# Kernel optimization log

Measured on AMD Instinct MI355X. Metric: run time of the kernel, lower is better.

## Reference

```python
import jax, jax.numpy as jnp
import numpy as np
from jax import lax

C, NORI, NROT, K, PAD = 256, 8, 2, 3, 1
B, H, W = 16, 64, 64
EPS = 1e-5


def setup_inputs() -> dict:
    key = jax.random.key(0)
    k1, k2, k3 = jax.random.split(key, 3)
    x = jax.random.normal(k1, (B, C, H, W), dtype=jnp.float32)
    # rotate_arf() output: [nRot*C, nOri*C, K, K]
    weight_all = jax.random.normal(k2, (NROT * C, NORI * C, K, K), dtype=jnp.float32) * 0.02
    bias_all = jax.random.normal(k3, (NROT * C,), dtype=jnp.float32) * 0.02
    alpha = jnp.float32(1.0)
    gamma = jnp.ones((C,), dtype=jnp.float32)
    beta = jnp.zeros((C,), dtype=jnp.float32)
    return {"x": x, "weight_all": weight_all, "bias_all": bias_all,
            "alpha": alpha, "gamma": gamma, "beta": beta}


def _forward(x, weight_all, bias_all, alpha, gamma, beta):
    # Loop of nOri*nRot convs over the same x with different weight blocks,
    # all accumulated into one [B,C,H,W] tensor == single conv with summed blocks
    # (conv is linear in the weights): fused form of the original loop.
    W_eff = weight_all.reshape(NROT, C, NORI, C, K, K).sum(axis=(0, 2))  # [C, C, K, K]
    b_eff = bias_all.reshape(NROT, C).sum(axis=0) * NORI                 # [C]
    d_sum = lax.conv_general_dilated(
        x, W_eff, window_strides=(1, 1), padding=[(PAD, PAD), (PAD, PAD)],
        dimension_numbers=("NCHW", "OIHW", "NCHW"))
    d_sum = d_sum + b_eff[None, :, None, None]
    d_mean = d_sum / float(NORI * NROT)
    out = x + alpha * d_mean
    # BatchNorm2d, training mode: biased batch stats over (B, H, W)
    mean = out.mean(axis=(0, 2, 3))
    var = ((out - mean[None, :, None, None]) ** 2).mean(axis=(0, 2, 3))
    inv = lax.rsqrt(var + EPS)
    y = (out - mean[None, :, None, None]) * (gamma * inv)[None, :, None, None] \
        + beta[None, :, None, None]
    return y


def reference(x, weight_all, bias_all, alpha, gamma, beta):
    return _forward(x, weight_all, bias_all, alpha, gamma, beta)
```

## Files before the change

kernel.cpp:

```cpp
#include <hip/hip_runtime.h>
#include <stdint.h>

typedef __attribute__((__ext_vector_type__(8))) __bf16 bf16x8;
typedef __attribute__((__ext_vector_type__(4))) float  f32x4;

#define XT_OFF    0ul
#define WT_OFF    33554432ul
#define BEFF_OFF  34734080ul
#define ZERO_OFF  34737152ul
#define STATS_OFF 34737408ul
#define V_OFF     35651584ul
#define WS_NEED   (V_OFF + 33554432ul)

__device__ inline void gload_lds16(const void* g, void* l) {
  __builtin_amdgcn_global_load_lds((const __attribute__((address_space(1))) void*)g,
                                   (__attribute__((address_space(3))) void*)l,
                                   16, 0, 0);
}

__global__ void k_prep(const float* __restrict__ w, const float* __restrict__ bias,
                       const float* __restrict__ alpha_p, __bf16* __restrict__ Wt,
                       float* __restrict__ beff, float* __restrict__ zerob,
                       float* __restrict__ statsG,
                       const float* __restrict__ x, __bf16* __restrict__ xT) {
  __shared__ __bf16 lds[64 * 258];
  if (blockIdx.x < 256) {
    const int co = blockIdx.x;
    const int ci = threadIdx.x;
    float a[9];
#pragma unroll
    for (int t = 0; t < 9; ++t) a[t] = 0.f;
#pragma unroll
    for (int r = 0; r < 2; ++r)
#pragma unroll
      for (int o = 0; o < 8; ++o) {
        const float* p = w + ((size_t)(r * 256 + co) * 2048 + (size_t)(o * 256 + ci)) * 9;
#pragma unroll
        for (int t = 0; t < 9; ++t) a[t] += p[t];
      }
    const float sc = alpha_p[0] * 0.0625f;
    const int s = ci >> 6, cis = ci & 63;
#pragma unroll
    for (int t = 0; t < 9; ++t)
      Wt[(size_t)(t * 4 + s) * 16384 + co * 64 + cis] = (__bf16)(a[t] * sc);
    if (ci == 0) beff[co] = (bias[co] + bias[256 + co]) * 8.0f * sc;
    if (blockIdx.x == 0) {
      statsG[ci] = 0.f; statsG[256 + ci] = 0.f;
      if (ci < 64) zerob[ci] = 0.f;
    }
  } else {
    int bh = blockIdx.x - 256;
    int b = bh >> 6, h = bh & 63;
    int t = threadIdx.x;
    int w2 = t & 63, cg = t >> 6;
    const float* xb = x + ((size_t)b * 16384 + h) * 64;
#pragma unroll 4
    for (int cb = 0; cb < 256; cb += 4) {
      int ci = cb + cg;
      lds[w2 * 258 + ci] = (__bf16)xb[(size_t)ci * 4096 + w2];
    }
    __syncthreads();
    const uint32_t* l32 = (const uint32_t*)lds;
    uint32_t* o32 = (uint32_t*)(xT + ((size_t)b * 64 + h) * 64 * 256);
    int c2 = t & 127, wg = t >> 7;
    for (int w0 = 0; w0 < 64; w0 += 2) {
      int ww = w0 + wg;
      o32[ww * 128 + c2] = l32[ww * 129 + c2];
    }
  }
}

#define A_BYTES 51200
#define B_BYTES 32768

__global__ __launch_bounds__(1024) void k_conv(
    const float* __restrict__ x, const __bf16* __restrict__ xT,
    const __bf16* __restrict__ Wt, const float* __restrict__ beff,
    const __bf16* __restrict__ zerob, float* __restrict__ out,
    float* __restrict__ statsG, __bf16* __restrict__ vout, int use_v16)
{
  __shared__ __align__(16) char lds[A_BYTES + 3 * B_BYTES + 2048];
  const int bb   = blockIdx.x >> 4;
  const int ho0  = (blockIdx.x & 15) << 2;
  const int tid  = threadIdx.x;
  const int lane = tid & 63;
  const int wid  = tid >> 6;
  const int wr   = wid >> 2;
  const int wc   = wid & 3;
  const int l15  = lane & 15;

  f32x4 acc[4][4];
#pragma unroll
  for (int i = 0; i < 4; ++i)
#pragma unroll
    for (int j = 0; j < 4; ++j)
#pragma unroll
      for (int r = 0; r < 4; ++r) acc[i][j][r] = 0.f;

  const char* zb = (const char*)zerob;

  int boff[4][2];
#pragma unroll
  for (int j = 0; j < 4; ++j)
#pragma unroll
    for (int kk = 0; kk < 2; ++kk) {
      const int co     = (wc << 6) + (j << 4) + l15;
      const int ci_off = (kk << 5) + ((lane >> 4) << 3);
      boff[j][kk] = ((co << 7) + (ci_off << 1)) ^ ((co & 7) << 4);
    }
  const int bl = lane >> 3;
  const int bsrcLane = (bl << 7) + (((lane & 7) ^ (bl & 7)) << 4);

  auto stageA = [&](int s) {
    const int ci0 = s << 6;
    for (int t = wid; t < 50; t += 16) {
      const int ch = (t << 3) + (lane >> 3);
      const int r  = ch / 66;
      const int c  = ch - r * 66;
      const int ir = ho0 - 1 + r;
      const int ic = c - 1;
      const int k  = (lane & 7) ^ (ch & 7);
      const char* src;
      if (ch < 396 && ir >= 0 && ir < 64 && ic >= 0 && ic < 64)
        src = (const char*)(xT + ((((size_t)bb << 6) + ir) * 64 + ic) * 256 + ci0 + (k << 3));
      else
        src = zb + (k << 4);
      gload_lds16(src, lds + (t << 10));
    }
  };

  auto stageB = [&](int ph, int bi) {
    char* buf = lds + A_BYTES + bi * B_BYTES;
    const int s2 = ph / 9, tp = ph - s2 * 9;
    const char* wsrc = (const char*)Wt + ((size_t)(tp * 4 + s2) << 15) + bsrcLane;
    gload_lds16(wsrc + (wid << 10), buf + (wid << 10));
    gload_lds16(wsrc + ((wid + 16) << 10), buf + ((wid + 16) << 10));
  };

  stageA(0);
  stageB(0, 0);
  stageB(1, 1);
  asm volatile("s_waitcnt vmcnt(0)" ::: "memory");
  __builtin_amdgcn_s_barrier();
  asm volatile("" ::: "memory");

  int s = 0, tap = 0, bcur = 0;
  for (int p = 0; p < 36; ++p) {
    if (p + 2 < 36) {
      int bnx = bcur + 2; if (bnx >= 3) bnx -= 3;
      stageB(p + 2, bnx);
    }
    const int dh = (tap >= 6) ? 2 : (tap >= 3 ? 1 : 0);
    const int dw = tap - dh * 3;
    const char* Bb = lds + A_BYTES + bcur * B_BYTES;
    __builtin_amdgcn_s_setprio(1);
#pragma unroll
    for (int kk = 0; kk < 2; ++kk) {
      const int ci_off = (kk << 5) + ((lane >> 4) << 3);
      bf16x8 av[4];
#pragma unroll
      for (int i = 0; i < 4; ++i) {
        const int pos = (wr + dh) * 66 + (i << 4) + l15 + dw;
        const int off = ((pos << 7) + (ci_off << 1)) ^ ((pos & 7) << 4);
        av[i] = *(const bf16x8*)(lds + off);
      }
#pragma unroll
      for (int j = 0; j < 4; ++j) {
        const bf16x8 bv = *(const bf16x8*)(Bb + boff[j][kk]);
#pragma unroll
        for (int i = 0; i < 4; ++i)
          acc[i][j] = __builtin_amdgcn_mfma_f32_16x16x32_bf16(av[i], bv, acc[i][j], 0, 0, 0);
      }
    }
    __builtin_amdgcn_s_setprio(0);

    if (tap == 8 && s < 3) {
      asm volatile("s_waitcnt vmcnt(0)" ::: "memory");
      __builtin_amdgcn_s_barrier();
      asm volatile("" ::: "memory");
      stageA(s + 1);
      asm volatile("s_waitcnt vmcnt(0)" ::: "memory");
      __builtin_amdgcn_s_barrier();
      asm volatile("" ::: "memory");
    } else if (p + 2 < 36) {
      asm volatile("s_waitcnt vmcnt(2)" ::: "memory");
      __builtin_amdgcn_s_barrier();
      asm volatile("" ::: "memory");
    } else if (p < 35) {
      asm volatile("s_waitcnt vmcnt(0)" ::: "memory");
      __builtin_amdgcn_s_barrier();
      asm volatile("" ::: "memory");
    }
    if (++tap == 9) { tap = 0; ++s; }
    if (++bcur == 3) bcur = 0;
  }

  __syncthreads();
  float* lstat = (float*)(lds + 32768);
  if (tid < 512) lstat[tid] = 0.f;
  __syncthreads();

  char* wreg = lds + wid * 2048;
  const int wq = lane >> 4;
  const int ho = ho0 + wr;
  const int xorco = (l15 & 7) << 4;
#pragma unroll
  for (int j = 0; j < 4; ++j) {
    const int co = (wc << 6) + (j << 4) + l15;
    const float be = beff[co];
    const size_t base = ((((size_t)bb << 8) + (size_t)co) << 12) + (ho << 6);
    float r1 = 0.f, r2 = 0.f;
#pragma unroll
    for (int i = 0; i < 4; ++i) {
      const int w0 = (i << 4) + (wq << 2);
      const float4 xv = *(const float4*)(x + base + w0);
      float4 v;
      v.x = acc[i][j][0] + xv.x + be;
      v.y = acc[i][j][1] + xv.y + be;
      v.z = acc[i][j][2] + xv.z + be;
      v.w = acc[i][j][3] + xv.w + be;
      r1 += v.x + v.y + v.z + v.w;
      r2 += v.x * v.x + v.y * v.y + v.z * v.z + v.w * v.w;
      if (use_v16) {
        union { __bf16 h[4]; uint64_t u; } pk;
        pk.h[0] = (__bf16)v.x; pk.h[1] = (__bf16)v.y;
        pk.h[2] = (__bf16)v.z; pk.h[3] = (__bf16)v.w;
        const int wa = (l15 << 7) + (i << 5) + (wq << 3);
        *(uint64_t*)(wreg + (wa ^ xorco)) = pk.u;
      } else {
        *(float4*)(out + base + w0) = v;
      }
    }
    r1 += __shfl_xor(r1, 16); r2 += __shfl_xor(r2, 16);
    r1 += __shfl_xor(r1, 32); r2 += __shfl_xor(r2, 32);
    if (lane < 16) {
      atomicAdd(&lstat[co], r1);
      atomicAdd(&lstat[256 + co], r2);
    }
    if (use_v16) {
      asm volatile("s_waitcnt lgkmcnt(0)" ::: "memory");
#pragma unroll
      for (int t2 = 0; t2 < 2; ++t2) {
        const int co_r = lane >> 2;
        const int ch   = (lane & 3) + (t2 << 2);
        const int ra   = (co_r << 7) + (ch << 4);
        const uint4 pv = *(const uint4*)(wreg + (ra ^ ((co_r & 7) << 4)));
        const int co_g = (wc << 6) + (j << 4) + co_r;
        const size_t oi = ((((size_t)bb << 8) + (size_t)co_g) << 12) + (ho << 6) + (ch << 3);
        *(uint4*)(vout + oi) = pv;
      }
      asm volatile("s_waitcnt lgkmcnt(0)" ::: "memory");
    }
  }
  __syncthreads();
  if (tid < 512) atomicAdd(&statsG[tid], lstat[tid]);
}

__global__ void k_apply_v16(const __bf16* __restrict__ v, float* __restrict__ out,
                            const float* __restrict__ statsG,
                            const float* __restrict__ gamma,
                            const float* __restrict__ beta) {
  __shared__ float ssc[256], ssh[256];
  const int t = threadIdx.x;
  {
    const float mean = statsG[t] * (1.f / 65536.f);
    const float var  = statsG[256 + t] * (1.f / 65536.f) - mean * mean;
    const float inv  = rsqrtf(var + 1e-5f);
    const float sc   = gamma[t] * inv;
    ssc[t] = sc;
    ssh[t] = beta[t] - mean * sc;
  }
  __syncthreads();
  const uint4* vp = (const uint4*)v;
  for (size_t g = (size_t)blockIdx.x * 256 + t; g < 2097152ul; g += (size_t)gridDim.x * 256) {
    const int co = (int)((g >> 9) & 255);
    const uint4 pv = vp[g];
    const float sc = ssc[co], sh = ssh[co];
    float4 y0, y1;
    y0.x = __uint_as_float((pv.x & 0xffffu) << 16) * sc + sh;
    y0.y = __uint_as_float(pv.x & 0xffff0000u) * sc + sh;
    y0.z = __uint_as_float((pv.y & 0xffffu) << 16) * sc + sh;
    y0.w = __uint_as_float(pv.y & 0xffff0000u) * sc + sh;
    y1.x = __uint_as_float((pv.z & 0xffffu) << 16) * sc + sh;
    y1.y = __uint_as_float(pv.z & 0xffff0000u) * sc + sh;
    y1.z = __uint_as_float((pv.w & 0xffffu) << 16) * sc + sh;
    y1.w = __uint_as_float(pv.w & 0xffff0000u) * sc + sh;
    float4* op = (float4*)(out + g * 8);
    op[0] = y0;
    op[1] = y1;
  }
}

__global__ void k_apply_f32(float* __restrict__ out, const float* __restrict__ statsG,
                            const float* __restrict__ gamma,
                            const float* __restrict__ beta) {
  __shared__ float ssc[256], ssh[256];
  const int t = threadIdx.x;
  {
    const float mean = statsG[t] * (1.f / 65536.f);
    const float var  = statsG[256 + t] * (1.f / 65536.f) - mean * mean;
    const float inv  = rsqrtf(var + 1e-5f);
    const float sc   = gamma[t] * inv;
    ssc[t] = sc;
    ssh[t] = beta[t] - mean * sc;
  }
  __syncthreads();
  float4* op = (float4*)out;
  for (size_t g = (size_t)blockIdx.x * 256 + t; g < 4194304ul; g += (size_t)gridDim.x * 256) {
    const int co = (int)((g >> 10) & 255);
    float4 y = op[g];
    const float sc = ssc[co], sh = ssh[co];
    y.x = y.x * sc + sh; y.y = y.y * sc + sh;
    y.z = y.z * sc + sh; y.w = y.w * sc + sh;
    op[g] = y;
  }
}

extern "C" void kernel_launch(void* const* d_in, const int* in_sizes, int n_in,
                              void* d_out, int out_size, void* d_ws, size_t ws_size,
                              hipStream_t stream) {
  const float* x     = (const float*)d_in[0];
  const float* wall  = (const float*)d_in[1];
  const float* bias  = (const float*)d_in[2];
  const float* alpha = (const float*)d_in[3];
  const float* gamma = (const float*)d_in[4];
  const float* beta  = (const float*)d_in[5];
  float* out = (float*)d_out;

  char* ws = (char*)d_ws;
  __bf16* xT     = (__bf16*)(ws + XT_OFF);
  __bf16* Wt     = (__bf16*)(ws + WT_OFF);
  float*  beff   = (float*)(ws + BEFF_OFF);
  float*  zerob  = (float*)(ws + ZERO_OFF);
  float*  statsG = (float*)(ws + STATS_OFF);
  __bf16* vbuf   = (__bf16*)(ws + V_OFF);
  const int use_v16 = (ws_size >= WS_NEED) ? 1 : 0;

  k_prep<<<1280, 256, 0, stream>>>(wall, bias, alpha, Wt, beff, zerob, statsG, x, xT);
  k_conv<<<256, 1024, 0, stream>>>(x, xT, Wt, beff, (const __bf16*)zerob, out,
                                   statsG, vbuf, use_v16);
  if (use_v16)
    k_apply_v16<<<2048, 256, 0, stream>>>(vbuf, out, statsG, gamma, beta);
  else
    k_apply_f32<<<2048, 256, 0, stream>>>(out, statsG, gamma, beta);
}
```

Measured before the change: 122.7 us.

## Split conv output channels across two 512-thread blocks, drop weight multi-buffering

The conv kernel now runs 512 blocks of 512 threads, each handling half of the 256 output channels for a 4-row tile. Adjacent block IDs are paired so both halves share the same input tile in cache. The triple-buffered weight prefetch is replaced by a single weight buffer that is loaded synchronously each tap. This shrinks LDS per block so more blocks can be resident and more of the GPU is used. The cost is that the input tile is loaded twice and global-load latency is no longer hidden behind the MFMA work.

```diff
diff --git a/kernel.cpp b/kernel.cpp
--- a/kernel.cpp
+++ b/kernel.cpp
@@ -71,22 +71,25 @@
 }
 
 #define A_BYTES 51200
-#define B_BYTES 32768
-
-__global__ __launch_bounds__(1024) void k_conv(
+#define B_BYTES 16384
+
+__global__ __launch_bounds__(512, 4) void k_conv(
     const float* __restrict__ x, const __bf16* __restrict__ xT,
     const __bf16* __restrict__ Wt, const float* __restrict__ beff,
     const __bf16* __restrict__ zerob, float* __restrict__ out,
     float* __restrict__ statsG, __bf16* __restrict__ vout, int use_v16)
 {
-  __shared__ __align__(16) char lds[A_BYTES + 3 * B_BYTES + 2048];
-  const int bb   = blockIdx.x >> 4;
-  const int ho0  = (blockIdx.x & 15) << 2;
+  __shared__ __align__(16) char lds[A_BYTES + B_BYTES + 1024];
+  const int u    = blockIdx.x;
+  const int ch   = (u >> 3) & 1;
+  const int pairid = (u & 7) | ((u >> 4) << 3);
+  const int bb   = pairid >> 4;
+  const int ho0  = (pairid & 15) << 2;
   const int tid  = threadIdx.x;
   const int lane = tid & 63;
   const int wid  = tid >> 6;
-  const int wr   = wid >> 2;
-  const int wc   = wid & 3;
+  const int wr   = wid >> 1;
+  const int wc   = wid & 1;
   const int l15  = lane & 15;
 
   f32x4 acc[4][4];
@@ -104,24 +107,24 @@
   for (int j = 0; j < 4; ++j)
 #pragma unroll
     for (int kk = 0; kk < 2; ++kk) {
-      const int co     = (wc << 6) + (j << 4) + l15;
+      const int col    = (wc << 6) + (j << 4) + l15;
       const int ci_off = (kk << 5) + ((lane >> 4) << 3);
-      boff[j][kk] = ((co << 7) + (ci_off << 1)) ^ ((co & 7) << 4);
+      boff[j][kk] = ((col << 7) + (ci_off << 1)) ^ ((col & 7) << 4);
     }
   const int bl = lane >> 3;
   const int bsrcLane = (bl << 7) + (((lane & 7) ^ (bl & 7)) << 4);
 
   auto stageA = [&](int s) {
     const int ci0 = s << 6;
-    for (int t = wid; t < 50; t += 16) {
-      const int ch = (t << 3) + (lane >> 3);
-      const int r  = ch / 66;
-      const int c  = ch - r * 66;
+    for (int t = wid; t < 50; t += 8) {
+      const int chk = (t << 3) + (lane >> 3);
+      const int r  = chk / 66;
+      const int c  = chk - r * 66;
       const int ir = ho0 - 1 + r;
       const int ic = c - 1;
-      const int k  = (lane & 7) ^ (ch & 7);
+      const int k  = (lane & 7) ^ (chk & 7);
       const char* src;
-      if (ch < 396 && ir >= 0 && ir < 64 && ic >= 0 && ic < 64)
+      if (chk < 396 && ir >= 0 && ir < 64 && ic >= 0 && ic < 64)
         src = (const char*)(xT + ((((size_t)bb << 6) + ir) * 64 + ic) * 256 + ci0 + (k << 3));
       else
         src = zb + (k << 4);
@@ -129,30 +132,25 @@
     }
   };
 
-  auto stageB = [&](int ph, int bi) {
-    char* buf = lds + A_BYTES + bi * B_BYTES;
+  auto stageB = [&](int ph) {
+    char* buf = lds + A_BYTES;
     const int s2 = ph / 9, tp = ph - s2 * 9;
-    const char* wsrc = (const char*)Wt + ((size_t)(tp * 4 + s2) << 15) + bsrcLane;
+    const char* wsrc = (const char*)Wt + ((size_t)(tp * 4 + s2) << 15) + (ch << 14) + bsrcLane;
     gload_lds16(wsrc + (wid << 10), buf + (wid << 10));
-    gload_lds16(wsrc + ((wid + 16) << 10), buf + ((wid + 16) << 10));
+    gload_lds16(wsrc + ((wid + 8) << 10), buf + ((wid + 8) << 10));
   };
 
-  stageA(0);
-  stageB(0, 0);
-  stageB(1, 1);
-  asm volatile("s_waitcnt vmcnt(0)" ::: "memory");
-  __builtin_amdgcn_s_barrier();
-  asm volatile("" ::: "memory");
-
-  int s = 0, tap = 0, bcur = 0;
+  int s = 0, tap = 0;
   for (int p = 0; p < 36; ++p) {
-    if (p + 2 < 36) {
-      int bnx = bcur + 2; if (bnx >= 3) bnx -= 3;
-      stageB(p + 2, bnx);
-    }
+    if (tap == 0) stageA(s);
+    stageB(p);
+    asm volatile("s_waitcnt vmcnt(0)" ::: "memory");
+    __builtin_amdgcn_s_barrier();
+    asm volatile("" ::: "memory");
+
     const int dh = (tap >= 6) ? 2 : (tap >= 3 ? 1 : 0);
     const int dw = tap - dh * 3;
-    const char* Bb = lds + A_BYTES + bcur * B_BYTES;
+    const char* Bb = lds + A_BYTES;
     __builtin_amdgcn_s_setprio(1);
 #pragma unroll
     for (int kk = 0; kk < 2; ++kk) {
@@ -173,31 +171,16 @@
       }
     }
     __builtin_amdgcn_s_setprio(0);
-
-    if (tap == 8 && s < 3) {
-      asm volatile("s_waitcnt vmcnt(0)" ::: "memory");
-      __builtin_amdgcn_s_barrier();
-      asm volatile("" ::: "memory");
-      stageA(s + 1);
-      asm volatile("s_waitcnt vmcnt(0)" ::: "memory");
-      __builtin_amdgcn_s_barrier();
-      asm volatile("" ::: "memory");
-    } else if (p + 2 < 36) {
-      asm volatile("s_waitcnt vmcnt(2)" ::: "memory");
-      __builtin_amdgcn_s_barrier();
-      asm volatile("" ::: "memory");
-    } else if (p < 35) {
-      asm volatile("s_waitcnt vmcnt(0)" ::: "memory");
-      __builtin_amdgcn_s_barrier();
-      asm volatile("" ::: "memory");
-    }
+    asm volatile("" ::: "memory");
+    __builtin_amdgcn_s_barrier();
+    asm volatile("" ::: "memory");
+
     if (++tap == 9) { tap = 0; ++s; }
-    if (++bcur == 3) bcur = 0;
-  }
-
-  __syncthreads();
-  float* lstat = (float*)(lds + 32768);
-  if (tid < 512) lstat[tid] = 0.f;
+  }
+
+  __syncthreads();
+  float* lstat = (float*)(lds + A_BYTES + B_BYTES);
+  if (tid < 256) lstat[tid] = 0.f;
   __syncthreads();
 
   char* wreg = lds + wid * 2048;
@@ -206,9 +189,10 @@
   const int xorco = (l15 & 7) << 4;
 #pragma unroll
   for (int j = 0; j < 4; ++j) {
-    const int co = (wc << 6) + (j << 4) + l15;
-    const float be = beff[co];
-    const size_t base = ((((size_t)bb << 8) + (size_t)co) << 12) + (ho << 6);
+    const int col = (wc << 6) + (j << 4) + l15;
+    const int cog = (ch << 7) + col;
+    const float be = beff[cog];
+    const size_t base = ((((size_t)bb << 8) + (size_t)cog) << 12) + (ho << 6);
     float r1 = 0.f, r2 = 0.f;
 #pragma unroll
     for (int i = 0; i < 4; ++i) {
@@ -222,11 +206,11 @@
       r1 += v.x + v.y + v.z + v.w;
       r2 += v.x * v.x + v.y * v.y + v.z * v.z + v.w * v.w;
       if (use_v16) {
-        union { __bf16 h[4]; uint64_t u; } pk;
+        union { __bf16 h[4]; uint64_t u64; } pk;
         pk.h[0] = (__bf16)v.x; pk.h[1] = (__bf16)v.y;
         pk.h[2] = (__bf16)v.z; pk.h[3] = (__bf16)v.w;
         const int wa = (l15 << 7) + (i << 5) + (wq << 3);
-        *(uint64_t*)(wreg + (wa ^ xorco)) = pk.u;
+        *(uint64_t*)(wreg + (wa ^ xorco)) = pk.u64;
       } else {
         *(float4*)(out + base + w0) = v;
       }
@@ -234,26 +218,29 @@
     r1 += __shfl_xor(r1, 16); r2 += __shfl_xor(r2, 16);
     r1 += __shfl_xor(r1, 32); r2 += __shfl_xor(r2, 32);
     if (lane < 16) {
-      atomicAdd(&lstat[co], r1);
-      atomicAdd(&lstat[256 + co], r2);
+      atomicAdd(&lstat[col], r1);
+      atomicAdd(&lstat[128 + col], r2);
     }
     if (use_v16) {
       asm volatile("s_waitcnt lgkmcnt(0)" ::: "memory");
 #pragma unroll
       for (int t2 = 0; t2 < 2; ++t2) {
         const int co_r = lane >> 2;
-        const int ch   = (lane & 3) + (t2 << 2);
-        const int ra   = (co_r << 7) + (ch << 4);
+        const int chk  = (lane & 3) + (t2 << 2);
+        const int ra   = (co_r << 7) + (chk << 4);
         const uint4 pv = *(const uint4*)(wreg + (ra ^ ((co_r & 7) << 4)));
-        const int co_g = (wc << 6) + (j << 4) + co_r;
-        const size_t oi = ((((size_t)bb << 8) + (size_t)co_g) << 12) + (ho << 6) + (ch << 3);
+        const int co_g = (ch << 7) + (wc << 6) + (j << 4) + co_r;
+        const size_t oi = ((((size_t)bb << 8) + (size_t)co_g) << 12) + (ho << 6) + (chk << 3);
         *(uint4*)(vout + oi) = pv;
       }
       asm volatile("s_waitcnt lgkmcnt(0)" ::: "memory");
     }
   }
   __syncthreads();
-  if (tid < 512) atomicAdd(&statsG[tid], lstat[tid]);
+  if (tid < 256) {
+    const int c = tid & 127, part = tid >> 7;
+    atomicAdd(&statsG[part * 256 + (ch << 7) + c], lstat[part * 128 + c]);
+  }
 }
 
 __global__ void k_apply_v16(const __bf16* __restrict__ v, float* __restrict__ out,
@@ -337,8 +324,8 @@
   const int use_v16 = (ws_size >= WS_NEED) ? 1 : 0;
 
   k_prep<<<1280, 256, 0, stream>>>(wall, bias, alpha, Wt, beff, zerob, statsG, x, xT);
-  k_conv<<<256, 1024, 0, stream>>>(x, xT, Wt, beff, (const __bf16*)zerob, out,
-                                   statsG, vbuf, use_v16);
+  k_conv<<<512, 512, 0, stream>>>(x, xT, Wt, beff, (const __bf16*)zerob, out,
+                                  statsG, vbuf, use_v16);
   if (use_v16)
     k_apply_v16<<<2048, 256, 0, stream>>>(vbuf, out, statsG, gamma, beta);
   else
```

Measured after the change: 115.7 us (median of 2 runs). -5.8%, faster.
